# Performance work log

Hardware: AMD Instinct MI355X
Metric: run time of the kernel (lower is better)

The kernel has to match this reference:

```python
import jax, jax.numpy as jnp
import numpy as np

B, L, D = 64, 1024, 64  # (batch*heads, seq_len, head_dim)


def setup_inputs() -> dict:
    key = jax.random.key(0)
    kq, kk, kv = jax.random.split(key, 3)
    q = jax.random.normal(kq, (B, L, D), dtype=jnp.float32)
    k = jax.random.normal(kk, (B, L, D), dtype=jnp.float32)
    v = jax.random.normal(kv, (B, L, D), dtype=jnp.float32)
    scale = jnp.float32(1.0 / np.sqrt(D))  # standard 1/sqrt(d_head)
    return {"q": q, "k": k, "v": v, "scale": scale}


def reference(q, k, v, scale):
    # attention = bmm(q, k^T) * scale  -> [B, L, L]
    attention = jnp.einsum("bqd,bkd->bqk", q, k) * scale
    # softmax over dim=2 (keys); dropout p=0.0 is identity
    attention = jax.nn.softmax(attention, axis=2)
    # context = bmm(attention, v) -> [B, L, D]
    context = jnp.einsum("bqk,bkd->bqd", attention, v)
    return (context, attention)
```

## Files before the change

### kernel.cpp

```cpp
#include <hip/hip_runtime.h>
#include <hip/hip_bf16.h>

typedef __bf16 bf16x8 __attribute__((ext_vector_type(8)));
typedef float  f32x4  __attribute__((ext_vector_type(4)));

#define NB 64
#define LL 1024
#define DD 64
#define PSTR 36

#define LDS_K_BYTES (LL * DD * 2)
#define LDS_TOTAL   (LDS_K_BYTES + 8 * 16 * PSTR * 4)

__global__ __launch_bounds__(256)
void preconvert_v(const float* __restrict__ v, __bf16* __restrict__ vt) {
  const int blk = blockIdx.x, tid = threadIdx.x;
  const int b = blk >> 4, t = blk & 15;
  __shared__ float tile[64][65];
  const float* src = v + ((size_t)b * LL + t * 64) * DD;
  for (int i = tid; i < 64 * 16; i += 256) {
    const int row = i >> 4, c4 = (i & 15) * 4;
    f32x4 x = *(const f32x4*)(src + row * DD + c4);
    tile[row][c4 + 0] = x[0]; tile[row][c4 + 1] = x[1];
    tile[row][c4 + 2] = x[2]; tile[row][c4 + 3] = x[3];
  }
  __syncthreads();
  __bf16* dst = vt + (size_t)b * DD * LL + t * 64;
  for (int i = tid; i < 64 * 8; i += 256) {
    const int d = i >> 3, k8 = (i & 7) * 8;
    bf16x8 o;
    #pragma unroll
    for (int j = 0; j < 8; ++j) o[j] = (__bf16)tile[k8 + j][d];
    *(bf16x8*)(dst + (size_t)d * LL + k8) = o;
  }
}

__global__ __launch_bounds__(512, 1)
void sdpa_resident(const float* __restrict__ q, const float* __restrict__ kf,
                   const __bf16* __restrict__ vt, const float* __restrict__ scale_p,
                   float* __restrict__ out) {
  extern __shared__ char smem[];
  __bf16* Klds = (__bf16*)smem;
  float*  Pw   = (float*)(smem + LDS_K_BYTES);

  const int tid  = threadIdx.x;
  const int lane = tid & 63;
  const int w    = tid >> 6;
  const int l15  = lane & 15;
  const int lg   = lane >> 4;

  int bid = blockIdx.x;
  bid = (bid & 7) * 32 + (bid >> 3);
  const int b     = bid >> 2;
  const int qrow0 = (bid & 3) * 256 + w * 32;

  const float scale = scale_p[0];
  const float* kb = kf + (size_t)b * LL * DD;
  const __bf16* vb = vt + (size_t)b * DD * LL;
  float* ctxb  = out + ((size_t)b * LL + qrow0) * DD;
  float* attnb = out + (size_t)NB * LL * DD + (size_t)b * LL * LL
               + (size_t)qrow0 * LL;

  #pragma unroll
  for (int it = 0; it < 16; ++it) {
    const int c = it * 512 + tid;
    const int row = c >> 3, slot = c & 7;
    const f32x4* s4 = (const f32x4*)(kb + (size_t)c * 8);
    f32x4 x0 = s4[0], x1 = s4[1];
    bf16x8 t;
    #pragma unroll
    for (int j = 0; j < 4; ++j) { t[j] = (__bf16)x0[j]; t[4 + j] = (__bf16)x1[j]; }
    *(bf16x8*)(Klds + row * 64 + ((slot * 8) ^ ((row & 7) * 8))) = t;
  }

  bf16x8 aq[2][2];
  #pragma unroll
  for (int u = 0; u < 2; ++u) {
    const float* qrow = q + ((size_t)b * LL + qrow0 + u * 16 + l15) * DD;
    #pragma unroll
    for (int s = 0; s < 2; ++s) {
      const f32x4* p4 = (const f32x4*)(qrow + s * 32 + lg * 8);
      f32x4 x0 = p4[0], x1 = p4[1];
      #pragma unroll
      for (int j = 0; j < 4; ++j) {
        aq[u][s][j]     = (__bf16)(x0[j] * scale);
        aq[u][s][4 + j] = (__bf16)(x1[j] * scale);
      }
    }
  }

  __syncthreads();

  const int xsw = (l15 & 7) * 8;

  float lsum[2] = {0.f, 0.f};
  for (int kt = 0; kt < LL / 32; ++kt) {
    bf16x8 bk[2][2];
    #pragma unroll
    for (int f = 0; f < 2; ++f)
      #pragma unroll
      for (int s = 0; s < 2; ++s)
        bk[f][s] = *(const bf16x8*)(Klds + (kt * 32 + f * 16 + l15) * 64
                                         + ((s * 32 + lg * 8) ^ xsw));
    #pragma unroll
    for (int u = 0; u < 2; ++u) {
      f32x4 sacc[2] = {{0.f,0.f,0.f,0.f},{0.f,0.f,0.f,0.f}};
      #pragma unroll
      for (int s = 0; s < 2; ++s)
        #pragma unroll
        for (int f = 0; f < 2; ++f)
          sacc[f] = __builtin_amdgcn_mfma_f32_16x16x32_bf16(bk[f][s], aq[u][s], sacc[f], 0, 0, 0);
      #pragma unroll
      for (int f = 0; f < 2; ++f)
        #pragma unroll
        for (int r = 0; r < 4; ++r)
          lsum[u] += __expf(sacc[f][r]);
    }
  }
  #pragma unroll
  for (int u = 0; u < 2; ++u) {
    lsum[u] += __shfl_xor(lsum[u], 16, 64);
    lsum[u] += __shfl_xor(lsum[u], 32, 64);
  }
  const float rl[2] = {1.0f / lsum[0], 1.0f / lsum[1]};

  f32x4 cacc[2][4];
  #pragma unroll
  for (int u = 0; u < 2; ++u)
    #pragma unroll
    for (int g = 0; g < 4; ++g)
      cacc[u][g] = (f32x4){0.f, 0.f, 0.f, 0.f};

  float* prow = Pw + (w * 16 + l15) * PSTR;

  bf16x8 bvn[4];
  #pragma unroll
  for (int g = 0; g < 4; ++g)
    bvn[g] = *(const bf16x8*)(vb + (size_t)(g * 16 + l15) * LL + lg * 8);

  for (int kt = 0; kt < LL / 32; ++kt) {
    bf16x8 bvc[4];
    #pragma unroll
    for (int g = 0; g < 4; ++g) bvc[g] = bvn[g];
    if (kt + 1 < LL / 32) {
      #pragma unroll
      for (int g = 0; g < 4; ++g)
        bvn[g] = *(const bf16x8*)(vb + (size_t)(g * 16 + l15) * LL
                                     + (kt + 1) * 32 + lg * 8);
    }

    bf16x8 bk[2][2];
    #pragma unroll
    for (int f = 0; f < 2; ++f)
      #pragma unroll
      for (int s = 0; s < 2; ++s)
        bk[f][s] = *(const bf16x8*)(Klds + (kt * 32 + f * 16 + l15) * 64
                                         + ((s * 32 + lg * 8) ^ xsw));

    #pragma unroll
    for (int u = 0; u < 2; ++u) {
      f32x4 sacc[2] = {{0.f,0.f,0.f,0.f},{0.f,0.f,0.f,0.f}};
      #pragma unroll
      for (int s = 0; s < 2; ++s)
        #pragma unroll
        for (int f = 0; f < 2; ++f)
          sacc[f] = __builtin_amdgcn_mfma_f32_16x16x32_bf16(bk[f][s], aq[u][s], sacc[f], 0, 0, 0);

      f32x4 pv[2];
      #pragma unroll
      for (int f = 0; f < 2; ++f)
        #pragma unroll
        for (int r = 0; r < 4; ++r)
          pv[f][r] = __expf(sacc[f][r]) * rl[u];

      float* arow = attnb + (size_t)(u * 16 + l15) * LL + kt * 32 + lg * 4;
      *(f32x4*)(arow)      = pv[0];
      *(f32x4*)(arow + 16) = pv[1];

      *(f32x4*)(prow + lg * 4)      = pv[0];
      *(f32x4*)(prow + 16 + lg * 4) = pv[1];
      f32x4 p0 = *(const f32x4*)(prow + lg * 8);
      f32x4 p1 = *(const f32x4*)(prow + lg * 8 + 4);
      bf16x8 pa;
      #pragma unroll
      for (int j = 0; j < 4; ++j) { pa[j] = (__bf16)p0[j]; pa[4 + j] = (__bf16)p1[j]; }

      #pragma unroll
      for (int g = 0; g < 4; ++g)
        cacc[u][g] = __builtin_amdgcn_mfma_f32_16x16x32_bf16(pa, bvc[g], cacc[u][g], 0, 0, 0);
    }
  }

  #pragma unroll
  for (int u = 0; u < 2; ++u)
    #pragma unroll
    for (int g = 0; g < 4; ++g)
      #pragma unroll
      for (int r = 0; r < 4; ++r)
        ctxb[(size_t)(u * 16 + lg * 4 + r) * DD + g * 16 + l15] = cacc[u][g][r];
}

#define BQ 64
#define BK 32
#define KSTRIDE 72
#define VSTRIDE 40
#define PSTRIDE 48

__global__ __launch_bounds__(256, 4)
void sdpa_fallback(const float* __restrict__ q, const float* __restrict__ k,
                   const float* __restrict__ v, const float* __restrict__ scale_p,
                   float* __restrict__ out) {
  const int tid  = threadIdx.x;
  const int lane = tid & 63;
  const int w    = tid >> 6;
  int bid = blockIdx.x;
  bid = (bid & 7) * 128 + (bid >> 3);
  const int b    = bid >> 4;
  const int qblk = (bid & 15) * BQ;

  __shared__ __bf16 Ks[BK * KSTRIDE];
  __shared__ __bf16 Vs[DD * VSTRIDE];
  __shared__ __bf16 Pp[4][16 * PSTRIDE];

  const float scale = scale_p[0];
  const float* qb = q + ((size_t)b * LL + qblk) * DD;
  const float* kb = k + (size_t)b * LL * DD;
  const float* vb = v + (size_t)b * LL * DD;
  float* ctx  = out + ((size_t)b * LL + qblk) * DD;
  float* attn = out + (size_t)NB * LL * DD + (size_t)b * LL * LL + (size_t)qblk * LL;

  const int l15 = lane & 15;
  const int lg  = lane >> 4;
  const int dchunk = lg * 8;

  bf16x8 aq[2];
  {
    const float* qrow = qb + (size_t)(w * 16 + l15) * DD;
    #pragma unroll
    for (int s = 0; s < 2; ++s) {
      const f32x4* p4 = (const f32x4*)(qrow + s * 32 + dchunk);
      f32x4 x0 = p4[0], x1 = p4[1];
      #pragma unroll
      for (int j = 0; j < 4; ++j) {
        aq[s][j]     = (__bf16)(x0[j] * scale);
        aq[s][4 + j] = (__bf16)(x1[j] * scale);
      }
    }
  }

  const int srow = tid >> 3;
  const int sd0  = (tid & 7) * 8;

  float lpart[4] = {0.f, 0.f, 0.f, 0.f};
  for (int kt = 0; kt < LL / BK; ++kt) {
    __syncthreads();
    {
      const f32x4* src = (const f32x4*)(kb + (size_t)(kt * BK + srow) * DD + sd0);
      f32x4 x0 = src[0], x1 = src[1];
      bf16x8 t;
      #pragma unroll
      for (int j = 0; j < 4; ++j) { t[j] = (__bf16)x0[j]; t[4 + j] = (__bf16)x1[j]; }
      *(bf16x8*)&Ks[srow * KSTRIDE + sd0] = t;
    }
    __syncthreads();
    f32x4 sacc[2] = {{0.f,0.f,0.f,0.f},{0.f,0.f,0.f,0.f}};
    #pragma unroll
    for (int s = 0; s < 2; ++s)
      #pragma unroll
      for (int f = 0; f < 2; ++f) {
        bf16x8 bk = *(const bf16x8*)&Ks[(f * 16 + l15) * KSTRIDE + s * 32 + dchunk];
        sacc[f] = __builtin_amdgcn_mfma_f32_16x16x32_bf16(aq[s], bk, sacc[f], 0, 0, 0);
      }
    #pragma unroll
    for (int f = 0; f < 2; ++f)
      #pragma unroll
      for (int r = 0; r < 4; ++r)
        lpart[r] += __expf(sacc[f][r]);
  }
  #pragma unroll
  for (int m = 1; m < 16; m <<= 1)
    #pragma unroll
    for (int r = 0; r < 4; ++r)
      lpart[r] += __shfl_xor(lpart[r], m, 64);
  float rl[4];
  #pragma unroll
  for (int r = 0; r < 4; ++r) rl[r] = 1.0f / lpart[r];

  f32x4 cacc[4] = {{0.f,0.f,0.f,0.f},{0.f,0.f,0.f,0.f},
                   {0.f,0.f,0.f,0.f},{0.f,0.f,0.f,0.f}};
  for (int kt = 0; kt < LL / BK; ++kt) {
    __syncthreads();
    {
      const f32x4* src = (const f32x4*)(kb + (size_t)(kt * BK + srow) * DD + sd0);
      f32x4 x0 = src[0], x1 = src[1];
      bf16x8 t;
      #pragma unroll
      for (int j = 0; j < 4; ++j) { t[j] = (__bf16)x0[j]; t[4 + j] = (__bf16)x1[j]; }
      *(bf16x8*)&Ks[srow * KSTRIDE + sd0] = t;
      const f32x4* vsrc = (const f32x4*)(vb + (size_t)(kt * BK + srow) * DD + sd0);
      f32x4 y0 = vsrc[0], y1 = vsrc[1];
      #pragma unroll
      for (int j = 0; j < 4; ++j) {
        Vs[(sd0 + j)     * VSTRIDE + srow] = (__bf16)y0[j];
        Vs[(sd0 + 4 + j) * VSTRIDE + srow] = (__bf16)y1[j];
      }
    }
    __syncthreads();
    f32x4 sacc[2] = {{0.f,0.f,0.f,0.f},{0.f,0.f,0.f,0.f}};
    #pragma unroll
    for (int s = 0; s < 2; ++s)
      #pragma unroll
      for (int f = 0; f < 2; ++f) {
        bf16x8 bk = *(const bf16x8*)&Ks[(f * 16 + l15) * KSTRIDE + s * 32 + dchunk];
        sacc[f] = __builtin_amdgcn_mfma_f32_16x16x32_bf16(aq[s], bk, sacc[f], 0, 0, 0);
      }
    #pragma unroll
    for (int f = 0; f < 2; ++f)
      #pragma unroll
      for (int r = 0; r < 4; ++r) {
        const int row = lg * 4 + r;
        float p = __expf(sacc[f][r]) * rl[r];
        attn[(size_t)(w * 16 + row) * LL + (kt * BK + f * 16 + l15)] = p;
        Pp[w][row * PSTRIDE + f * 16 + l15] = (__bf16)p;
      }
    bf16x8 pa = *(const bf16x8*)&Pp[w][l15 * PSTRIDE + lg * 8];
    #pragma unroll
    for (int g = 0; g < 4; ++g) {
      bf16x8 bv = *(const bf16x8*)&Vs[(g * 16 + l15) * VSTRIDE + lg * 8];
      cacc[g] = __builtin_amdgcn_mfma_f32_16x16x32_bf16(pa, bv, cacc[g], 0, 0, 0);
    }
  }
  #pragma unroll
  for (int g = 0; g < 4; ++g)
    #pragma unroll
    for (int r = 0; r < 4; ++r)
      ctx[(size_t)(w * 16 + lg * 4 + r) * DD + g * 16 + l15] = cacc[g][r];
}

extern "C" void kernel_launch(void* const* d_in, const int* in_sizes, int n_in,
                              void* d_out, int out_size, void* d_ws, size_t ws_size,
                              hipStream_t stream) {
  const float* q = (const float*)d_in[0];
  const float* k = (const float*)d_in[1];
  const float* v = (const float*)d_in[2];
  const float* s = (const float*)d_in[3];
  float* out = (float*)d_out;

  const size_t vbytes = (size_t)NB * LL * DD * 2;
  if (ws_size >= vbytes) {
    __bf16* vt = (__bf16*)d_ws;
    preconvert_v<<<dim3(NB * (LL / 64)), dim3(256), 0, stream>>>(v, vt);
    (void)hipFuncSetAttribute((const void*)sdpa_resident,
                              hipFuncAttributeMaxDynamicSharedMemorySize,
                              LDS_TOTAL);
    sdpa_resident<<<dim3(256), dim3(512), LDS_TOTAL, stream>>>(q, k, vt, s, out);
  } else {
    sdpa_fallback<<<dim3(NB * (LL / 64)), dim3(256), 0, stream>>>(q, k, v, s, out);
  }
}
```

Before: 109.7 us.

## Split softmax row-sum pass into separate high-occupancy kernel with bf16 K preconversion

Preconverts K to bf16 in the same preprocessing kernel as V. Moves the first pass (computing softmax denominators) into its own kernel with 512 blocks of 256 threads, reading K from global memory with register double-buffering, and stores reciprocal sums to workspace. The main kernel then loads bf16 K into LDS and reads the precomputed reciprocals. This aims to raise occupancy and parallelism for the exp-sum pass, which previously ran on only 256 single-occupancy blocks. In exchange it adds kernel launches and extra global traffic for the converted K and the row sums.

Result: slower. 135.1 us (+23.2%).

```diff
diff --git a/kernel.cpp b/kernel.cpp
--- a/kernel.cpp
+++ b/kernel.cpp
@@ -12,37 +12,48 @@
 #define LDS_K_BYTES (LL * DD * 2)
 #define LDS_TOTAL   (LDS_K_BYTES + 8 * 16 * PSTR * 4)
 
+#define WS_VT_OFF 0
+#define WS_KB_OFF ((size_t)8 * 1024 * 1024)
+#define WS_RL_OFF ((size_t)16 * 1024 * 1024)
+#define WS_NEED   (WS_RL_OFF + (size_t)NB * LL * 4)
+
 __global__ __launch_bounds__(256)
-void preconvert_v(const float* __restrict__ v, __bf16* __restrict__ vt) {
+void preconvert_kv(const float* __restrict__ k, const float* __restrict__ v,
+                   __bf16* __restrict__ kbf, __bf16* __restrict__ vt) {
   const int blk = blockIdx.x, tid = threadIdx.x;
-  const int b = blk >> 4, t = blk & 15;
-  __shared__ float tile[64][65];
-  const float* src = v + ((size_t)b * LL + t * 64) * DD;
-  for (int i = tid; i < 64 * 16; i += 256) {
-    const int row = i >> 4, c4 = (i & 15) * 4;
-    f32x4 x = *(const f32x4*)(src + row * DD + c4);
-    tile[row][c4 + 0] = x[0]; tile[row][c4 + 1] = x[1];
-    tile[row][c4 + 2] = x[2]; tile[row][c4 + 3] = x[3];
-  }
-  __syncthreads();
-  __bf16* dst = vt + (size_t)b * DD * LL + t * 64;
-  for (int i = tid; i < 64 * 8; i += 256) {
-    const int d = i >> 3, k8 = (i & 7) * 8;
+  if (blk < NB * (LL / 64)) {
+    const int b = blk >> 4, t = blk & 15;
+    __shared__ float tile[64][65];
+    const float* src = v + ((size_t)b * LL + t * 64) * DD;
+    for (int i = tid; i < 64 * 16; i += 256) {
+      const int row = i >> 4, c4 = (i & 15) * 4;
+      f32x4 x = *(const f32x4*)(src + row * DD + c4);
+      tile[row][c4 + 0] = x[0]; tile[row][c4 + 1] = x[1];
+      tile[row][c4 + 2] = x[2]; tile[row][c4 + 3] = x[3];
+    }
+    __syncthreads();
+    __bf16* dst = vt + (size_t)b * DD * LL + t * 64;
+    for (int i = tid; i < 64 * 8; i += 256) {
+      const int d = i >> 3, k8 = (i & 7) * 8;
+      bf16x8 o;
+      #pragma unroll
+      for (int j = 0; j < 8; ++j) o[j] = (__bf16)tile[k8 + j][d];
+      *(bf16x8*)(dst + (size_t)d * LL + k8) = o;
+    }
+  } else {
+    const size_t base = ((size_t)(blk - 1024) * 256 + tid) * 8;
+    const f32x4* s = (const f32x4*)(k + base);
+    f32x4 x0 = s[0], x1 = s[1];
     bf16x8 o;
     #pragma unroll
-    for (int j = 0; j < 8; ++j) o[j] = (__bf16)tile[k8 + j][d];
-    *(bf16x8*)(dst + (size_t)d * LL + k8) = o;
+    for (int j = 0; j < 4; ++j) { o[j] = (__bf16)x0[j]; o[4 + j] = (__bf16)x1[j]; }
+    *(bf16x8*)(kbf + base) = o;
   }
 }
 
-__global__ __launch_bounds__(512, 1)
-void sdpa_resident(const float* __restrict__ q, const float* __restrict__ kf,
-                   const __bf16* __restrict__ vt, const float* __restrict__ scale_p,
-                   float* __restrict__ out) {
-  extern __shared__ char smem[];
-  __bf16* Klds = (__bf16*)smem;
-  float*  Pw   = (float*)(smem + LDS_K_BYTES);
-
+__global__ __launch_bounds__(256, 4)
+void lsum_kernel(const float* __restrict__ q, const __bf16* __restrict__ kbf,
+                 const float* __restrict__ scale_p, float* __restrict__ rlbuf) {
   const int tid  = threadIdx.x;
   const int lane = tid & 63;
   const int w    = tid >> 6;
@@ -50,33 +61,17 @@
   const int lg   = lane >> 4;
 
   int bid = blockIdx.x;
-  bid = (bid & 7) * 32 + (bid >> 3);
-  const int b     = bid >> 2;
-  const int qrow0 = (bid & 3) * 256 + w * 32;
+  bid = (bid & 7) * 64 + (bid >> 3);
+  const int b     = bid >> 3;
+  const int qbase = (bid & 7) * 128 + w * 32;
 
   const float scale = scale_p[0];
-  const float* kb = kf + (size_t)b * LL * DD;
-  const __bf16* vb = vt + (size_t)b * DD * LL;
-  float* ctxb  = out + ((size_t)b * LL + qrow0) * DD;
-  float* attnb = out + (size_t)NB * LL * DD + (size_t)b * LL * LL
-               + (size_t)qrow0 * LL;
-
-  #pragma unroll
-  for (int it = 0; it < 16; ++it) {
-    const int c = it * 512 + tid;
-    const int row = c >> 3, slot = c & 7;
-    const f32x4* s4 = (const f32x4*)(kb + (size_t)c * 8);
-    f32x4 x0 = s4[0], x1 = s4[1];
-    bf16x8 t;
-    #pragma unroll
-    for (int j = 0; j < 4; ++j) { t[j] = (__bf16)x0[j]; t[4 + j] = (__bf16)x1[j]; }
-    *(bf16x8*)(Klds + row * 64 + ((slot * 8) ^ ((row & 7) * 8))) = t;
-  }
+  const __bf16* kb = kbf + (size_t)b * LL * DD;
 
   bf16x8 aq[2][2];
   #pragma unroll
   for (int u = 0; u < 2; ++u) {
-    const float* qrow = q + ((size_t)b * LL + qrow0 + u * 16 + l15) * DD;
+    const float* qrow = q + ((size_t)b * LL + qbase + u * 16 + l15) * DD;
     #pragma unroll
     for (int s = 0; s < 2; ++s) {
       const f32x4* p4 = (const f32x4*)(qrow + s * 32 + lg * 8);
@@ -89,19 +84,29 @@
     }
   }
 
-  __syncthreads();
-
-  const int xsw = (l15 & 7) * 8;
+  bf16x8 nk[2][2];
+  #pragma unroll
+  for (int f = 0; f < 2; ++f)
+    #pragma unroll
+    for (int s = 0; s < 2; ++s)
+      nk[f][s] = *(const bf16x8*)(kb + (size_t)(f * 16 + l15) * DD + s * 32 + lg * 8);
 
   float lsum[2] = {0.f, 0.f};
   for (int kt = 0; kt < LL / 32; ++kt) {
-    bf16x8 bk[2][2];
+    bf16x8 ck[2][2];
     #pragma unroll
     for (int f = 0; f < 2; ++f)
       #pragma unroll
       for (int s = 0; s < 2; ++s)
-        bk[f][s] = *(const bf16x8*)(Klds + (kt * 32 + f * 16 + l15) * 64
-                                         + ((s * 32 + lg * 8) ^ xsw));
+        ck[f][s] = nk[f][s];
+    if (kt + 1 < LL / 32) {
+      const __bf16* kp = kb + (size_t)(kt + 1) * 32 * DD;
+      #pragma unroll
+      for (int f = 0; f < 2; ++f)
+        #pragma unroll
+        for (int s = 0; s < 2; ++s)
+          nk[f][s] = *(const bf16x8*)(kp + (size_t)(f * 16 + l15) * DD + s * 32 + lg * 8);
+    }
     #pragma unroll
     for (int u = 0; u < 2; ++u) {
       f32x4 sacc[2] = {{0.f,0.f,0.f,0.f},{0.f,0.f,0.f,0.f}};
@@ -109,7 +114,7 @@
       for (int s = 0; s < 2; ++s)
         #pragma unroll
         for (int f = 0; f < 2; ++f)
-          sacc[f] = __builtin_amdgcn_mfma_f32_16x16x32_bf16(bk[f][s], aq[u][s], sacc[f], 0, 0, 0);
+          sacc[f] = __builtin_amdgcn_mfma_f32_16x16x32_bf16(ck[f][s], aq[u][s], sacc[f], 0, 0, 0);
       #pragma unroll
       for (int f = 0; f < 2; ++f)
         #pragma unroll
@@ -122,7 +127,68 @@
     lsum[u] += __shfl_xor(lsum[u], 16, 64);
     lsum[u] += __shfl_xor(lsum[u], 32, 64);
   }
-  const float rl[2] = {1.0f / lsum[0], 1.0f / lsum[1]};
+  if (lg == 0) {
+    float* rp = rlbuf + (size_t)b * LL + qbase + l15;
+    rp[0]  = 1.0f / lsum[0];
+    rp[16] = 1.0f / lsum[1];
+  }
+}
+
+__global__ __launch_bounds__(512, 1)
+void sdpa_pass2(const float* __restrict__ q, const __bf16* __restrict__ kbf,
+                const __bf16* __restrict__ vt, const float* __restrict__ rlbuf,
+                const float* __restrict__ scale_p, float* __restrict__ out) {
+  extern __shared__ char smem[];
+  __bf16* Klds = (__bf16*)smem;
+  float*  Pw   = (float*)(smem + LDS_K_BYTES);
+
+  const int tid  = threadIdx.x;
+  const int lane = tid & 63;
+  const int w    = tid >> 6;
+  const int l15  = lane & 15;
+  const int lg   = lane >> 4;
+
+  int bid = blockIdx.x;
+  bid = (bid & 7) * 32 + (bid >> 3);
+  const int b     = bid >> 2;
+  const int qrow0 = (bid & 3) * 256 + w * 32;
+
+  const float scale = scale_p[0];
+  const __bf16* kb = kbf + (size_t)b * LL * DD;
+  const __bf16* vb = vt  + (size_t)b * DD * LL;
+  float* ctxb  = out + ((size_t)b * LL + qrow0) * DD;
+  float* attnb = out + (size_t)NB * LL * DD + (size_t)b * LL * LL
+               + (size_t)qrow0 * LL;
+
+  #pragma unroll
+  for (int it = 0; it < 16; ++it) {
+    const int c = it * 512 + tid;
+    const int row = c >> 3, slot = c & 7;
+    bf16x8 t = *(const bf16x8*)(kb + (size_t)c * 8);
+    *(bf16x8*)(Klds + row * 64 + ((slot * 8) ^ ((row & 7) * 8))) = t;
+  }
+
+  bf16x8 aq[2][2];
+  #pragma unroll
+  for (int u = 0; u < 2; ++u) {
+    const float* qrow = q + ((size_t)b * LL + qrow0 + u * 16 + l15) * DD;
+    #pragma unroll
+    for (int s = 0; s < 2; ++s) {
+      const f32x4* p4 = (const f32x4*)(qrow + s * 32 + lg * 8);
+      f32x4 x0 = p4[0], x1 = p4[1];
+      #pragma unroll
+      for (int j = 0; j < 4; ++j) {
+        aq[u][s][j]     = (__bf16)(x0[j] * scale);
+        aq[u][s][4 + j] = (__bf16)(x1[j] * scale);
+      }
+    }
+  }
+  const float* rlp = rlbuf + (size_t)b * LL + qrow0 + l15;
+  const float rl[2] = {rlp[0], rlp[16]};
+
+  __syncthreads();
+
+  const int xsw = (l15 & 7) * 8;
 
   f32x4 cacc[2][4];
   #pragma unroll
@@ -346,14 +412,16 @@
   const float* s = (const float*)d_in[3];
   float* out = (float*)d_out;
 
-  const size_t vbytes = (size_t)NB * LL * DD * 2;
-  if (ws_size >= vbytes) {
-    __bf16* vt = (__bf16*)d_ws;
-    preconvert_v<<<dim3(NB * (LL / 64)), dim3(256), 0, stream>>>(v, vt);
-    (void)hipFuncSetAttribute((const void*)sdpa_resident,
+  if (ws_size >= WS_NEED) {
+    __bf16* vt  = (__bf16*)((char*)d_ws + WS_VT_OFF);
+    __bf16* kbf = (__bf16*)((char*)d_ws + WS_KB_OFF);
+    float*  rl  = (float*)((char*)d_ws + WS_RL_OFF);
+    preconvert_kv<<<dim3(3072), dim3(256), 0, stream>>>(k, v, kbf, vt);
+    lsum_kernel<<<dim3(512), dim3(256), 0, stream>>>(q, kbf, s, rl);
+    (void)hipFuncSetAttribute((const void*)sdpa_pass2,
                               hipFuncAttributeMaxDynamicSharedMemorySize,
                               LDS_TOTAL);
-    sdpa_resident<<<dim3(256), dim3(512), LDS_TOTAL, stream>>>(q, k, vt, s, out);
+    sdpa_pass2<<<dim3(256), dim3(512), LDS_TOTAL, stream>>>(q, kbf, vt, rl, s, out);
   } else {
     sdpa_fallback<<<dim3(NB * (LL / 64)), dim3(256), 0, stream>>>(q, k, v, s, out);
   }
```

## Pipeline row-sum pass of second subtile into first subtile's output pass, use exp2

Applied to the files above, without the earlier changes.

The two 16-row subtiles per wave are no longer processed in lockstep. The first subtile's row sums are computed in a dedicated pass, then its output pass also computes the second subtile's row sums, and a final pass emits the second subtile. This removes one full QK^T sweep (three sweeps instead of four). The log2(e) factor is folded into the Q scale so native exp2 replaces expf. The P staging buffer in LDS becomes bf16, halving its traffic. The cost is extra MFMA work inside the middle loop and more register pressure.

Measured after the change: 107.3 us (median of 2 runs). 2.2% less time.

```diff
diff --git a/kernel.cpp b/kernel.cpp
--- a/kernel.cpp
+++ b/kernel.cpp
@@ -2,15 +2,22 @@
 #include <hip/hip_bf16.h>
 
 typedef __bf16 bf16x8 __attribute__((ext_vector_type(8)));
+typedef __bf16 bf16x4 __attribute__((ext_vector_type(4)));
 typedef float  f32x4  __attribute__((ext_vector_type(4)));
 
 #define NB 64
 #define LL 1024
 #define DD 64
-#define PSTR 36
+#define PB 40
 
 #define LDS_K_BYTES (LL * DD * 2)
-#define LDS_TOTAL   (LDS_K_BYTES + 8 * 16 * PSTR * 4)
+#define LDS_TOTAL   (LDS_K_BYTES + 8 * 16 * PB * 2)
+
+#if __has_builtin(__builtin_amdgcn_exp2f)
+#define EXP2(x) __builtin_amdgcn_exp2f(x)
+#else
+#define EXP2(x) exp2f(x)
+#endif
 
 __global__ __launch_bounds__(256)
 void preconvert_v(const float* __restrict__ v, __bf16* __restrict__ vt) {
@@ -36,12 +43,12 @@
 }
 
 __global__ __launch_bounds__(512, 1)
-void sdpa_resident(const float* __restrict__ q, const float* __restrict__ kf,
-                   const __bf16* __restrict__ vt, const float* __restrict__ scale_p,
-                   float* __restrict__ out) {
+void sdpa_fused(const float* __restrict__ q, const float* __restrict__ kf,
+                const __bf16* __restrict__ vt, const float* __restrict__ scale_p,
+                float* __restrict__ out) {
   extern __shared__ char smem[];
   __bf16* Klds = (__bf16*)smem;
-  float*  Pw   = (float*)(smem + LDS_K_BYTES);
+  __bf16* Pw   = (__bf16*)(smem + LDS_K_BYTES);
 
   const int tid  = threadIdx.x;
   const int lane = tid & 63;
@@ -54,7 +61,7 @@
   const int b     = bid >> 2;
   const int qrow0 = (bid & 3) * 256 + w * 32;
 
-  const float scale = scale_p[0];
+  const float scale2 = scale_p[0] * 1.4426950408889634f;
   const float* kb = kf + (size_t)b * LL * DD;
   const __bf16* vb = vt + (size_t)b * DD * LL;
   float* ctxb  = out + ((size_t)b * LL + qrow0) * DD;
@@ -83,8 +90,8 @@
       f32x4 x0 = p4[0], x1 = p4[1];
       #pragma unroll
       for (int j = 0; j < 4; ++j) {
-        aq[u][s][j]     = (__bf16)(x0[j] * scale);
-        aq[u][s][4 + j] = (__bf16)(x1[j] * scale);
+        aq[u][s][j]     = (__bf16)(x0[j] * scale2);
+        aq[u][s][4 + j] = (__bf16)(x1[j] * scale2);
       }
     }
   }
@@ -92,8 +99,9 @@
   __syncthreads();
 
   const int xsw = (l15 & 7) * 8;
-
-  float lsum[2] = {0.f, 0.f};
+  __bf16* prow = Pw + (w * 16 + l15) * PB;
+
+  float ls0 = 0.f;
   for (int kt = 0; kt < LL / 32; ++kt) {
     bf16x8 bk[2][2];
     #pragma unroll
@@ -102,36 +110,29 @@
       for (int s = 0; s < 2; ++s)
         bk[f][s] = *(const bf16x8*)(Klds + (kt * 32 + f * 16 + l15) * 64
                                          + ((s * 32 + lg * 8) ^ xsw));
-    #pragma unroll
-    for (int u = 0; u < 2; ++u) {
-      f32x4 sacc[2] = {{0.f,0.f,0.f,0.f},{0.f,0.f,0.f,0.f}};
-      #pragma unroll
-      for (int s = 0; s < 2; ++s)
-        #pragma unroll
-        for (int f = 0; f < 2; ++f)
-          sacc[f] = __builtin_amdgcn_mfma_f32_16x16x32_bf16(bk[f][s], aq[u][s], sacc[f], 0, 0, 0);
+    f32x4 sacc[2] = {{0.f,0.f,0.f,0.f},{0.f,0.f,0.f,0.f}};
+    #pragma unroll
+    for (int s = 0; s < 2; ++s)
       #pragma unroll
       for (int f = 0; f < 2; ++f)
-        #pragma unroll
-        for (int r = 0; r < 4; ++r)
-          lsum[u] += __expf(sacc[f][r]);
-    }
-  }
-  #pragma unroll
-  for (int u = 0; u < 2; ++u) {
-    lsum[u] += __shfl_xor(lsum[u], 16, 64);
-    lsum[u] += __shfl_xor(lsum[u], 32, 64);
-  }
-  const float rl[2] = {1.0f / lsum[0], 1.0f / lsum[1]};
-
-  f32x4 cacc[2][4];
-  #pragma unroll
-  for (int u = 0; u < 2; ++u)
-    #pragma unroll
-    for (int g = 0; g < 4; ++g)
-      cacc[u][g] = (f32x4){0.f, 0.f, 0.f, 0.f};
-
-  float* prow = Pw + (w * 16 + l15) * PSTR;
+        sacc[f] = __builtin_amdgcn_mfma_f32_16x16x32_bf16(bk[f][s], aq[0][s], sacc[f], 0, 0, 0);
+    #pragma unroll
+    for (int f = 0; f < 2; ++f)
+      #pragma unroll
+      for (int r = 0; r < 4; ++r)
+        ls0 += EXP2(sacc[f][r]);
+  }
+  ls0 += __shfl_xor(ls0, 16, 64);
+  ls0 += __shfl_xor(ls0, 32, 64);
+  const float rl0 = 1.0f / ls0;
+
+  f32x4 cacc0[4], cacc1[4];
+  #pragma unroll
+  for (int g = 0; g < 4; ++g) {
+    cacc0[g] = (f32x4){0.f, 0.f, 0.f, 0.f};
+    cacc1[g] = (f32x4){0.f, 0.f, 0.f, 0.f};
+  }
+  float ls1 = 0.f;
 
   bf16x8 bvn[4];
   #pragma unroll
@@ -157,47 +158,110 @@
         bk[f][s] = *(const bf16x8*)(Klds + (kt * 32 + f * 16 + l15) * 64
                                          + ((s * 32 + lg * 8) ^ xsw));
 
-    #pragma unroll
-    for (int u = 0; u < 2; ++u) {
-      f32x4 sacc[2] = {{0.f,0.f,0.f,0.f},{0.f,0.f,0.f,0.f}};
+    f32x4 s0[2] = {{0.f,0.f,0.f,0.f},{0.f,0.f,0.f,0.f}};
+    f32x4 s1[2] = {{0.f,0.f,0.f,0.f},{0.f,0.f,0.f,0.f}};
+    #pragma unroll
+    for (int s = 0; s < 2; ++s)
+      #pragma unroll
+      for (int f = 0; f < 2; ++f) {
+        s0[f] = __builtin_amdgcn_mfma_f32_16x16x32_bf16(bk[f][s], aq[0][s], s0[f], 0, 0, 0);
+        s1[f] = __builtin_amdgcn_mfma_f32_16x16x32_bf16(bk[f][s], aq[1][s], s1[f], 0, 0, 0);
+      }
+
+    f32x4 pv[2];
+    #pragma unroll
+    for (int f = 0; f < 2; ++f)
+      #pragma unroll
+      for (int r = 0; r < 4; ++r)
+        pv[f][r] = EXP2(s0[f][r]) * rl0;
+
+    float* arow = attnb + (size_t)l15 * LL + kt * 32 + lg * 4;
+    *(f32x4*)(arow)      = pv[0];
+    *(f32x4*)(arow + 16) = pv[1];
+
+    #pragma unroll
+    for (int f = 0; f < 2; ++f) {
+      bf16x4 pb;
+      #pragma unroll
+      for (int r = 0; r < 4; ++r) pb[r] = (__bf16)pv[f][r];
+      *(bf16x4*)(prow + f * 16 + lg * 4) = pb;
+    }
+    bf16x8 pa = *(const bf16x8*)(prow + lg * 8);
+    #pragma unroll
+    for (int g = 0; g < 4; ++g)
+      cacc0[g] = __builtin_amdgcn_mfma_f32_16x16x32_bf16(pa, bvc[g], cacc0[g], 0, 0, 0);
+
+    #pragma unroll
+    for (int f = 0; f < 2; ++f)
+      #pragma unroll
+      for (int r = 0; r < 4; ++r)
+        ls1 += EXP2(s1[f][r]);
+  }
+  ls1 += __shfl_xor(ls1, 16, 64);
+  ls1 += __shfl_xor(ls1, 32, 64);
+  const float rl1 = 1.0f / ls1;
+
+  #pragma unroll
+  for (int g = 0; g < 4; ++g)
+    bvn[g] = *(const bf16x8*)(vb + (size_t)(g * 16 + l15) * LL + lg * 8);
+
+  for (int kt = 0; kt < LL / 32; ++kt) {
+    bf16x8 bvc[4];
+    #pragma unroll
+    for (int g = 0; g < 4; ++g) bvc[g] = bvn[g];
+    if (kt + 1 < LL / 32) {
+      #pragma unroll
+      for (int g = 0; g < 4; ++g)
+        bvn[g] = *(const bf16x8*)(vb + (size_t)(g * 16 + l15) * LL
+                                     + (kt + 1) * 32 + lg * 8);
+    }
+
+    bf16x8 bk[2][2];
+    #pragma unroll
+    for (int f = 0; f < 2; ++f)
       #pragma unroll
       for (int s = 0; s < 2; ++s)
-        #pragma unroll
-        for (int f = 0; f < 2; ++f)
-          sacc[f] = __builtin_amdgcn_mfma_f32_16x16x32_bf16(bk[f][s], aq[u][s], sacc[f], 0, 0, 0);
-
-      f32x4 pv[2];
+        bk[f][s] = *(const bf16x8*)(Klds + (kt * 32 + f * 16 + l15) * 64
+                                         + ((s * 32 + lg * 8) ^ xsw));
+
+    f32x4 s1[2] = {{0.f,0.f,0.f,0.f},{0.f,0.f,0.f,0.f}};
+    #pragma unroll
+    for (int s = 0; s < 2; ++s)
       #pragma unroll
       for (int f = 0; f < 2; ++f)
-        #pragma unroll
-        for (int r = 0; r < 4; ++r)
-          pv[f][r] = __expf(sacc[f][r]) * rl[u];
-
-      float* arow = attnb + (size_t)(u * 16 + l15) * LL + kt * 32 + lg * 4;
-      *(f32x4*)(arow)      = pv[0];
-      *(f32x4*)(arow + 16) = pv[1];
-
-      *(f32x4*)(prow + lg * 4)      = pv[0];
-      *(f32x4*)(prow + 16 + lg * 4) = pv[1];
-      f32x4 p0 = *(const f32x4*)(prow + lg * 8);
-      f32x4 p1 = *(const f32x4*)(prow + lg * 8 + 4);
-      bf16x8 pa;
-      #pragma unroll
-      for (int j = 0; j < 4; ++j) { pa[j] = (__bf16)p0[j]; pa[4 + j] = (__bf16)p1[j]; }
-
-      #pragma unroll
-      for (int g = 0; g < 4; ++g)
-        cacc[u][g] = __builtin_amdgcn_mfma_f32_16x16x32_bf16(pa, bvc[g], cacc[u][g], 0, 0, 0);
-    }
-  }
-
-  #pragma unroll
-  for (int u = 0; u < 2; ++u)
+        s1[f] = __builtin_amdgcn_mfma_f32_16x16x32_bf16(bk[f][s], aq[1][s], s1[f], 0, 0, 0);
+
+    f32x4 pv[2];
+    #pragma unroll
+    for (int f = 0; f < 2; ++f)
+      #pragma unroll
+      for (int r = 0; r < 4; ++r)
+        pv[f][r] = EXP2(s1[f][r]) * rl1;
+
+    float* arow = attnb + (size_t)(16 + l15) * LL + kt * 32 + lg * 4;
+    *(f32x4*)(arow)      = pv[0];
+    *(f32x4*)(arow + 16) = pv[1];
+
+    #pragma unroll
+    for (int f = 0; f < 2; ++f) {
+      bf16x4 pb;
+      #pragma unroll
+      for (int r = 0; r < 4; ++r) pb[r] = (__bf16)pv[f][r];
+      *(bf16x4*)(prow + f * 16 + lg * 4) = pb;
+    }
+    bf16x8 pa = *(const bf16x8*)(prow + lg * 8);
     #pragma unroll
     for (int g = 0; g < 4; ++g)
-      #pragma unroll
-      for (int r = 0; r < 4; ++r)
-        ctxb[(size_t)(u * 16 + lg * 4 + r) * DD + g * 16 + l15] = cacc[u][g][r];
+      cacc1[g] = __builtin_amdgcn_mfma_f32_16x16x32_bf16(pa, bvc[g], cacc1[g], 0, 0, 0);
+  }
+
+  #pragma unroll
+  for (int g = 0; g < 4; ++g)
+    #pragma unroll
+    for (int r = 0; r < 4; ++r) {
+      ctxb[(size_t)(lg * 4 + r) * DD + g * 16 + l15]        = cacc0[g][r];
+      ctxb[(size_t)(16 + lg * 4 + r) * DD + g * 16 + l15]   = cacc1[g][r];
+    }
 }
 
 #define BQ 64
@@ -350,10 +414,10 @@
   if (ws_size >= vbytes) {
     __bf16* vt = (__bf16*)d_ws;
     preconvert_v<<<dim3(NB * (LL / 64)), dim3(256), 0, stream>>>(v, vt);
-    (void)hipFuncSetAttribute((const void*)sdpa_resident,
+    (void)hipFuncSetAttribute((const void*)sdpa_fused,
                               hipFuncAttributeMaxDynamicSharedMemorySize,
                               LDS_TOTAL);
-    sdpa_resident<<<dim3(256), dim3(512), LDS_TOTAL, stream>>>(q, k, vt, s, out);
+    sdpa_fused<<<dim3(256), dim3(512), LDS_TOTAL, stream>>>(q, k, vt, s, out);
   } else {
     sdpa_fallback<<<dim3(NB * (LL / 64)), dim3(256), 0, stream>>>(q, k, v, s, out);
   }
```

## Widen resident SDPA block to 16 waves with staggered key tiles and bf16 P staging

Applied to the files above, without the earlier changes.

The resident kernel now runs 1024 threads (16 waves) per block, each wave handling 16 query rows instead of 32, which doubles the waves available to hide latency per CU. Each wave starts its key-tile loop at a different offset to spread LDS and global access. It also uses exp2 with the log2e folded into the scale, stages P in LDS as bf16 instead of fp32, prefetches V two tiles ahead, and writes the attention matrix with nontemporal stores. The cost is more register pressure per thread under the 1024-thread bound, and QK^T still has to be computed twice.

New measurement: 123.2 us. +12.4%, slower.

```diff
diff --git a/kernel.cpp b/kernel.cpp
--- a/kernel.cpp
+++ b/kernel.cpp
@@ -2,15 +2,23 @@
 #include <hip/hip_bf16.h>
 
 typedef __bf16 bf16x8 __attribute__((ext_vector_type(8)));
+typedef __bf16 bf16x4 __attribute__((ext_vector_type(4)));
 typedef float  f32x4  __attribute__((ext_vector_type(4)));
 
 #define NB 64
 #define LL 1024
 #define DD 64
-#define PSTR 36
-
+#define PB 40
+
+#define NW 16
 #define LDS_K_BYTES (LL * DD * 2)
-#define LDS_TOTAL   (LDS_K_BYTES + 8 * 16 * PSTR * 4)
+#define LDS_TOTAL   (LDS_K_BYTES + NW * 16 * PB * 2)
+
+#if __has_builtin(__builtin_amdgcn_exp2f)
+#define EXP2(x) __builtin_amdgcn_exp2f(x)
+#else
+#define EXP2(x) exp2f(x)
+#endif
 
 __global__ __launch_bounds__(256)
 void preconvert_v(const float* __restrict__ v, __bf16* __restrict__ vt) {
@@ -35,13 +43,13 @@
   }
 }
 
-__global__ __launch_bounds__(512, 1)
-void sdpa_resident(const float* __restrict__ q, const float* __restrict__ kf,
-                   const __bf16* __restrict__ vt, const float* __restrict__ scale_p,
-                   float* __restrict__ out) {
+__global__ __launch_bounds__(1024, 1)
+void sdpa_wide(const float* __restrict__ q, const float* __restrict__ kf,
+               const __bf16* __restrict__ vt, const float* __restrict__ scale_p,
+               float* __restrict__ out) {
   extern __shared__ char smem[];
   __bf16* Klds = (__bf16*)smem;
-  float*  Pw   = (float*)(smem + LDS_K_BYTES);
+  __bf16* Pw   = (__bf16*)(smem + LDS_K_BYTES);
 
   const int tid  = threadIdx.x;
   const int lane = tid & 63;
@@ -52,9 +60,9 @@
   int bid = blockIdx.x;
   bid = (bid & 7) * 32 + (bid >> 3);
   const int b     = bid >> 2;
-  const int qrow0 = (bid & 3) * 256 + w * 32;
-
-  const float scale = scale_p[0];
+  const int qrow0 = (bid & 3) * 256 + w * 16;
+
+  const float scale2 = scale_p[0] * 1.4426950408889634f;
   const float* kb = kf + (size_t)b * LL * DD;
   const __bf16* vb = vt + (size_t)b * DD * LL;
   float* ctxb  = out + ((size_t)b * LL + qrow0) * DD;
@@ -62,8 +70,8 @@
                + (size_t)qrow0 * LL;
 
   #pragma unroll
-  for (int it = 0; it < 16; ++it) {
-    const int c = it * 512 + tid;
+  for (int it = 0; it < 8; ++it) {
+    const int c = it * 1024 + tid;
     const int row = c >> 3, slot = c & 7;
     const f32x4* s4 = (const f32x4*)(kb + (size_t)c * 8);
     f32x4 x0 = s4[0], x1 = s4[1];
@@ -73,131 +81,124 @@
     *(bf16x8*)(Klds + row * 64 + ((slot * 8) ^ ((row & 7) * 8))) = t;
   }
 
-  bf16x8 aq[2][2];
-  #pragma unroll
-  for (int u = 0; u < 2; ++u) {
-    const float* qrow = q + ((size_t)b * LL + qrow0 + u * 16 + l15) * DD;
+  bf16x8 aq[2];
+  {
+    const float* qrow = q + ((size_t)b * LL + qrow0 + l15) * DD;
     #pragma unroll
     for (int s = 0; s < 2; ++s) {
       const f32x4* p4 = (const f32x4*)(qrow + s * 32 + lg * 8);
       f32x4 x0 = p4[0], x1 = p4[1];
       #pragma unroll
       for (int j = 0; j < 4; ++j) {
-        aq[u][s][j]     = (__bf16)(x0[j] * scale);
-        aq[u][s][4 + j] = (__bf16)(x1[j] * scale);
+        aq[s][j]     = (__bf16)(x0[j] * scale2);
+        aq[s][4 + j] = (__bf16)(x1[j] * scale2);
       }
     }
   }
 
   __syncthreads();
 
-  const int xsw = (l15 & 7) * 8;
-
-  float lsum[2] = {0.f, 0.f};
-  for (int kt = 0; kt < LL / 32; ++kt) {
+  const int xsw  = (l15 & 7) * 8;
+  const int woff = (w * 2) & 31;
+  __bf16* prow = Pw + (w * 16 + l15) * PB;
+
+  float ls = 0.f;
+  for (int kt = 0; kt < 32; ++kt) {
+    const int kk = (kt + woff) & 31;
     bf16x8 bk[2][2];
     #pragma unroll
     for (int f = 0; f < 2; ++f)
       #pragma unroll
       for (int s = 0; s < 2; ++s)
-        bk[f][s] = *(const bf16x8*)(Klds + (kt * 32 + f * 16 + l15) * 64
+        bk[f][s] = *(const bf16x8*)(Klds + (kk * 32 + f * 16 + l15) * 64
                                          + ((s * 32 + lg * 8) ^ xsw));
-    #pragma unroll
-    for (int u = 0; u < 2; ++u) {
-      f32x4 sacc[2] = {{0.f,0.f,0.f,0.f},{0.f,0.f,0.f,0.f}};
+    f32x4 sacc[2] = {{0.f,0.f,0.f,0.f},{0.f,0.f,0.f,0.f}};
+    #pragma unroll
+    for (int s = 0; s < 2; ++s)
+      #pragma unroll
+      for (int f = 0; f < 2; ++f)
+        sacc[f] = __builtin_amdgcn_mfma_f32_16x16x32_bf16(bk[f][s], aq[s], sacc[f], 0, 0, 0);
+    #pragma unroll
+    for (int f = 0; f < 2; ++f)
+      #pragma unroll
+      for (int r = 0; r < 4; ++r)
+        ls += EXP2(sacc[f][r]);
+  }
+  ls += __shfl_xor(ls, 16, 64);
+  ls += __shfl_xor(ls, 32, 64);
+  const float rl = 1.0f / ls;
+
+  f32x4 cacc[4];
+  #pragma unroll
+  for (int g = 0; g < 4; ++g) cacc[g] = (f32x4){0.f, 0.f, 0.f, 0.f};
+
+  bf16x8 bvA[4], bvB[4];
+  {
+    const int k0 = woff, k1 = (woff + 1) & 31;
+    #pragma unroll
+    for (int g = 0; g < 4; ++g) {
+      bvA[g] = *(const bf16x8*)(vb + (size_t)(g * 16 + l15) * LL + k0 * 32 + lg * 8);
+      bvB[g] = *(const bf16x8*)(vb + (size_t)(g * 16 + l15) * LL + k1 * 32 + lg * 8);
+    }
+  }
+
+  for (int kt = 0; kt < 32; ++kt) {
+    const int kk  = (kt + woff) & 31;
+    const int kk2 = (kt + 2 + woff) & 31;
+
+    bf16x8 bvc[4];
+    #pragma unroll
+    for (int g = 0; g < 4; ++g) bvc[g] = bvA[g];
+    #pragma unroll
+    for (int g = 0; g < 4; ++g) bvA[g] = bvB[g];
+    #pragma unroll
+    for (int g = 0; g < 4; ++g)
+      bvB[g] = *(const bf16x8*)(vb + (size_t)(g * 16 + l15) * LL + kk2 * 32 + lg * 8);
+
+    bf16x8 bk[2][2];
+    #pragma unroll
+    for (int f = 0; f < 2; ++f)
       #pragma unroll
       for (int s = 0; s < 2; ++s)
-        #pragma unroll
-        for (int f = 0; f < 2; ++f)
-          sacc[f] = __builtin_amdgcn_mfma_f32_16x16x32_bf16(bk[f][s], aq[u][s], sacc[f], 0, 0, 0);
+        bk[f][s] = *(const bf16x8*)(Klds + (kk * 32 + f * 16 + l15) * 64
+                                         + ((s * 32 + lg * 8) ^ xsw));
+
+    f32x4 sacc[2] = {{0.f,0.f,0.f,0.f},{0.f,0.f,0.f,0.f}};
+    #pragma unroll
+    for (int s = 0; s < 2; ++s)
       #pragma unroll
       for (int f = 0; f < 2; ++f)
-        #pragma unroll
-        for (int r = 0; r < 4; ++r)
-          lsum[u] += __expf(sacc[f][r]);
-    }
-  }
-  #pragma unroll
-  for (int u = 0; u < 2; ++u) {
-    lsum[u] += __shfl_xor(lsum[u], 16, 64);
-    lsum[u] += __shfl_xor(lsum[u], 32, 64);
-  }
-  const float rl[2] = {1.0f / lsum[0], 1.0f / lsum[1]};
-
-  f32x4 cacc[2][4];
-  #pragma unroll
-  for (int u = 0; u < 2; ++u)
+        sacc[f] = __builtin_amdgcn_mfma_f32_16x16x32_bf16(bk[f][s], aq[s], sacc[f], 0, 0, 0);
+
+    f32x4 pv[2];
+    #pragma unroll
+    for (int f = 0; f < 2; ++f)
+      #pragma unroll
+      for (int r = 0; r < 4; ++r)
+        pv[f][r] = EXP2(sacc[f][r]) * rl;
+
+    #pragma unroll
+    for (int f = 0; f < 2; ++f) {
+      bf16x4 pb;
+      #pragma unroll
+      for (int r = 0; r < 4; ++r) pb[r] = (__bf16)pv[f][r];
+      *(bf16x4*)(prow + f * 16 + lg * 4) = pb;
+    }
+    bf16x8 pa = *(const bf16x8*)(prow + lg * 8);
     #pragma unroll
     for (int g = 0; g < 4; ++g)
-      cacc[u][g] = (f32x4){0.f, 0.f, 0.f, 0.f};
-
-  float* prow = Pw + (w * 16 + l15) * PSTR;
-
-  bf16x8 bvn[4];
+      cacc[g] = __builtin_amdgcn_mfma_f32_16x16x32_bf16(pa, bvc[g], cacc[g], 0, 0, 0);
+
+    float* arow = attnb + (size_t)l15 * LL + kk * 32 + lg * 4;
+    __builtin_nontemporal_store(pv[0], (f32x4*)arow);
+    __builtin_nontemporal_store(pv[1], (f32x4*)(arow + 16));
+  }
+
   #pragma unroll
   for (int g = 0; g < 4; ++g)
-    bvn[g] = *(const bf16x8*)(vb + (size_t)(g * 16 + l15) * LL + lg * 8);
-
-  for (int kt = 0; kt < LL / 32; ++kt) {
-    bf16x8 bvc[4];
-    #pragma unroll
-    for (int g = 0; g < 4; ++g) bvc[g] = bvn[g];
-    if (kt + 1 < LL / 32) {
-      #pragma unroll
-      for (int g = 0; g < 4; ++g)
-        bvn[g] = *(const bf16x8*)(vb + (size_t)(g * 16 + l15) * LL
-                                     + (kt + 1) * 32 + lg * 8);
-    }
-
-    bf16x8 bk[2][2];
-    #pragma unroll
-    for (int f = 0; f < 2; ++f)
-      #pragma unroll
-      for (int s = 0; s < 2; ++s)
-        bk[f][s] = *(const bf16x8*)(Klds + (kt * 32 + f * 16 + l15) * 64
-                                         + ((s * 32 + lg * 8) ^ xsw));
-
-    #pragma unroll
-    for (int u = 0; u < 2; ++u) {
-      f32x4 sacc[2] = {{0.f,0.f,0.f,0.f},{0.f,0.f,0.f,0.f}};
-      #pragma unroll
-      for (int s = 0; s < 2; ++s)
-        #pragma unroll
-        for (int f = 0; f < 2; ++f)
-          sacc[f] = __builtin_amdgcn_mfma_f32_16x16x32_bf16(bk[f][s], aq[u][s], sacc[f], 0, 0, 0);
-
-      f32x4 pv[2];
-      #pragma unroll
-      for (int f = 0; f < 2; ++f)
-        #pragma unroll
-        for (int r = 0; r < 4; ++r)
-          pv[f][r] = __expf(sacc[f][r]) * rl[u];
-
-      float* arow = attnb + (size_t)(u * 16 + l15) * LL + kt * 32 + lg * 4;
-      *(f32x4*)(arow)      = pv[0];
-      *(f32x4*)(arow + 16) = pv[1];
-
-      *(f32x4*)(prow + lg * 4)      = pv[0];
-      *(f32x4*)(prow + 16 + lg * 4) = pv[1];
-      f32x4 p0 = *(const f32x4*)(prow + lg * 8);
-      f32x4 p1 = *(const f32x4*)(prow + lg * 8 + 4);
-      bf16x8 pa;
-      #pragma unroll
-      for (int j = 0; j < 4; ++j) { pa[j] = (__bf16)p0[j]; pa[4 + j] = (__bf16)p1[j]; }
-
-      #pragma unroll
-      for (int g = 0; g < 4; ++g)
-        cacc[u][g] = __builtin_amdgcn_mfma_f32_16x16x32_bf16(pa, bvc[g], cacc[u][g], 0, 0, 0);
-    }
-  }
-
-  #pragma unroll
-  for (int u = 0; u < 2; ++u)
-    #pragma unroll
-    for (int g = 0; g < 4; ++g)
-      #pragma unroll
-      for (int r = 0; r < 4; ++r)
-        ctxb[(size_t)(u * 16 + lg * 4 + r) * DD + g * 16 + l15] = cacc[u][g][r];
+    #pragma unroll
+    for (int r = 0; r < 4; ++r)
+      ctxb[(size_t)(lg * 4 + r) * DD + g * 16 + l15] = cacc[g][r];
 }
 
 #define BQ 64
@@ -350,10 +351,10 @@
   if (ws_size >= vbytes) {
     __bf16* vt = (__bf16*)d_ws;
     preconvert_v<<<dim3(NB * (LL / 64)), dim3(256), 0, stream>>>(v, vt);
-    (void)hipFuncSetAttribute((const void*)sdpa_resident,
+    (void)hipFuncSetAttribute((const void*)sdpa_wide,
                               hipFuncAttributeMaxDynamicSharedMemorySize,
                               LDS_TOTAL);
-    sdpa_resident<<<dim3(256), dim3(512), LDS_TOTAL, stream>>>(q, k, vt, s, out);
+    sdpa_wide<<<dim3(256), dim3(1024), LDS_TOTAL, stream>>>(q, k, vt, s, out);
   } else {
     sdpa_fallback<<<dim3(NB * (LL / 64)), dim3(256), 0, stream>>>(q, k, v, s, out);
   }
```
